# Kernel optimization log

Measured on AMD Instinct MI355X. Metric: run time of the kernel, lower is better.

The kernel has to match this reference:

```python
import jax, jax.numpy as jnp
import numpy as np

B, S, H, F, V, MAX_OOV = 128, 512, 1024, 512, 50000, 50


def setup_inputs() -> dict:
    key = jax.random.key(0)
    ks = jax.random.split(key, 20)
    r = lambda i, shp, s=0.02: (jax.random.normal(ks[i], shp, jnp.float32) * s)
    return dict(
        input=jax.random.randint(ks[0], (B,), 0, V),
        hidden=jax.random.normal(ks[1], (1, B, H), jnp.float32) * 0.1,
        encoder_outputs=jax.random.normal(ks[2], (B, S, H), jnp.float32) * 0.1,
        x_padding_masks=jnp.ones((B, S), jnp.float32),
        len_oov=jax.random.randint(ks[3], (B,), 0, MAX_OOV),
        coverage_vector=jnp.zeros((B, S), jnp.float32),
        ref2tgt=jax.random.randint(ks[4], (B, S), 0, V + MAX_OOV),
        emb=r(5, (V, F)),
        W_ih=r(6, (3 * H, F)), W_hh=r(7, (3 * H, H)),
        b_ih=jnp.zeros(3 * H, jnp.float32), b_hh=jnp.zeros(3 * H, jnp.float32),
        e2v1_w=r(8, (F, H)), e2v1_b=jnp.zeros(F, jnp.float32),
        e2v2_w=r(9, (V, F)), e2v2_b=jnp.zeros(V, jnp.float32),
        fc_w=r(10, (H, 2 * H)), fc_b=jnp.zeros(H, jnp.float32),
        wgen_w=r(11, (1, 2 * H + F)), wgen_b=jnp.zeros(1, jnp.float32),
        att_Wh=r(12, (H, H)), att_Ws=r(13, (H, H)),
        att_wc=r(14, (H,)), att_b=jnp.zeros(H, jnp.float32), att_v=r(15, (H,)),
    )


def reference(input, hidden, encoder_outputs, x_padding_masks, len_oov,
              coverage_vector, ref2tgt, emb, W_ih, W_hh, b_ih, b_hh,
              e2v1_w, e2v1_b, e2v2_w, e2v2_b, fc_w, fc_b, wgen_w, wgen_b,
              att_Wh, att_Ws, att_wc, att_b, att_v):
    # embedding lookup (dropout is identity at inference)
    emb_x = emb[input]  # [B, F]

    # --- additive (Bahdanau) attention with coverage ---
    s = hidden[0]  # [B, H] (n_layers == 1)
    feat = jnp.tanh(
        jnp.einsum('bsh,kh->bsk', encoder_outputs, att_Wh)
        + (s @ att_Ws.T)[:, None, :]
        + coverage_vector[:, :, None] * att_wc
        + att_b)  # [B, S, H]
    e = jnp.einsum('bsh,h->bs', feat, att_v)  # [B, S]
    a = jax.nn.softmax(e, axis=1) * x_padding_masks
    a = a / (jnp.sum(a, axis=1, keepdims=True))  # [B, S] renormalized attn
    coverage_new = coverage_vector + a
    context = jnp.einsum('bs,bsh->bh', a, encoder_outputs)  # [B, H]
    h_att = jnp.concatenate([s, context], axis=-1) @ fc_w.T + fc_b  # [B, H]

    # --- single-step GRU (PyTorch gate order r, z, n) ---
    gi = emb_x @ W_ih.T + b_ih  # [B, 3H]
    gh = h_att @ W_hh.T + b_hh  # [B, 3H]
    i_r, i_z, i_n = jnp.split(gi, 3, axis=-1)
    h_r, h_z, h_n = jnp.split(gh, 3, axis=-1)
    r = jax.nn.sigmoid(i_r + h_r)
    z = jax.nn.sigmoid(i_z + h_z)
    n = jnp.tanh(i_n + r * h_n)
    h_new = (1.0 - z) * n + z * h_att  # [B, H]

    # --- vocab distribution ---
    out1 = h_new @ e2v1_w.T + e2v1_b  # [B, F]
    p_vocab = jax.nn.softmax(out1 @ e2v2_w.T + e2v2_b, axis=1)  # [B, V]

    # --- pointer-generator mixing ---
    x_gen = jnp.concatenate([context, h_new, emb_x], axis=-1)  # [B, 2H+F]
    p_gen = jax.nn.sigmoid(x_gen @ wgen_w.T + wgen_b)[:, 0]  # [B]
    p_gen = jnp.clip(p_gen, 0.001, 0.999)
    p_vocab_w = p_gen[:, None] * p_vocab  # [B, V]
    attn_w = (1.0 - p_gen)[:, None] * a  # [B, S]
    p_ext = jnp.concatenate([p_vocab_w, jnp.zeros((B, MAX_OOV), p_vocab_w.dtype)], axis=1)
    rows = jnp.arange(B)[:, None]
    final = p_ext.at[rows, ref2tgt].add(attn_w)  # scatter_add over extended vocab

    return final, h_new[None], coverage_new, a
```

## Files before the change

### kernel.cpp

```cpp
#include <hip/hip_runtime.h>
#include <math.h>

#define B_   128
#define S_   512
#define H_   1024
#define F_   512
#define V_   50000
#define OOV_ 50
#define EV_  (V_ + OOV_)

#define BM 128
#define BN 128
#define BK 64

typedef __attribute__((ext_vector_type(8))) __bf16 bf16x8;
typedef __attribute__((ext_vector_type(4))) __bf16 bf16x4;
typedef __attribute__((ext_vector_type(4))) float  f32x4;

__device__ __forceinline__ void gload_lds16(const void* g, void* lds) {
  __builtin_amdgcn_global_load_lds(
      (const __attribute__((address_space(1))) unsigned int*)g,
      (__attribute__((address_space(3))) unsigned int*)lds, 16, 0, 0);
}

__device__ __forceinline__ float fast_tanh(float x) {
  float v = fminf(fmaxf(x, -15.f), 15.f);
  float t = __expf(2.f * v);
  return 1.f - 2.f / (t + 1.f);
}

__global__ __launch_bounds__(256)
void cast_both_kernel(const float* __restrict__ enc, __bf16* __restrict__ enc_h,
                      const float* __restrict__ wh, __bf16* __restrict__ wh_h)
{
  const size_t n_enc = (size_t)B_ * S_ * H_;
  const size_t n_tot = n_enc + (size_t)H_ * H_;
  for (size_t i = ((size_t)blockIdx.x * 256 + threadIdx.x) * 8; i < n_tot;
       i += (size_t)gridDim.x * 256 * 8) {
    const float* in; __bf16* out; size_t j;
    if (i < n_enc) { in = enc; out = enc_h; j = i; }
    else           { in = wh;  out = wh_h;  j = i - n_enc; }
    float4 a = *(const float4*)(in + j);
    float4 b = *(const float4*)(in + j + 4);
    bf16x8 o;
    o[0] = (__bf16)a.x; o[1] = (__bf16)a.y; o[2] = (__bf16)a.z; o[3] = (__bf16)a.w;
    o[4] = (__bf16)b.x; o[5] = (__bf16)b.y; o[6] = (__bf16)b.z; o[7] = (__bf16)b.w;
    *(bf16x8*)(out + j) = o;
  }
}

__global__ __launch_bounds__(256)
void gemm_splitk(const float* __restrict__ A, const float* __restrict__ W,
                 float* __restrict__ partial, int N, int K, int KS)
{
  __shared__ float As[128 * 68];
  __shared__ float Ws[32 * 68];
  const int tid = threadIdx.x;
  const int n0 = blockIdx.x * 32;
  const int p  = blockIdx.y;
  const int tx = tid & 7, ty = tid >> 3;
  const int lr = tid >> 4, lc4 = (tid & 15) * 4;
  float acc[4][4] = {};
  const int kend = p * KS + KS;
  for (int k0 = p * KS; k0 < kend; k0 += 64) {
#pragma unroll
    for (int pp = 0; pp < 8; ++pp)
      *(float4*)(As + (pp * 16 + lr) * 68 + lc4) =
          *(const float4*)(A + (size_t)(pp * 16 + lr) * K + k0 + lc4);
#pragma unroll
    for (int pp = 0; pp < 2; ++pp)
      *(float4*)(Ws + (pp * 16 + lr) * 68 + lc4) =
          *(const float4*)(W + (size_t)(n0 + pp * 16 + lr) * K + k0 + lc4);
    __syncthreads();
#pragma unroll
    for (int kk = 0; kk < 16; ++kk) {
      float4 av[4], wv[4];
#pragma unroll
      for (int i = 0; i < 4; i++) av[i] = *(const float4*)(As + (ty * 4 + i) * 68 + kk * 4);
#pragma unroll
      for (int j = 0; j < 4; j++) wv[j] = *(const float4*)(Ws + (tx * 4 + j) * 68 + kk * 4);
#pragma unroll
      for (int i = 0; i < 4; i++)
#pragma unroll
        for (int j = 0; j < 4; j++) {
          acc[i][j] = fmaf(av[i].x, wv[j].x, acc[i][j]);
          acc[i][j] = fmaf(av[i].y, wv[j].y, acc[i][j]);
          acc[i][j] = fmaf(av[i].z, wv[j].z, acc[i][j]);
          acc[i][j] = fmaf(av[i].w, wv[j].w, acc[i][j]);
        }
    }
    __syncthreads();
  }
#pragma unroll
  for (int i = 0; i < 4; i++)
#pragma unroll
    for (int j = 0; j < 4; j++)
      partial[((size_t)p * 128 + ty * 4 + i) * N + n0 + tx * 4 + j] = acc[i][j];
}

__global__ __launch_bounds__(256)
void gemm_splitk_cat(const float* __restrict__ A1, const float* __restrict__ A2,
                     const float* __restrict__ W, float* __restrict__ partial,
                     int N, int K, int KS)
{
  __shared__ float As[128 * 68];
  __shared__ float Ws[32 * 68];
  const int tid = threadIdx.x;
  const int n0 = blockIdx.x * 32;
  const int p  = blockIdx.y;
  const int tx = tid & 7, ty = tid >> 3;
  const int lr = tid >> 4, lc4 = (tid & 15) * 4;
  const float* A = (p * KS < 1024) ? A1 : A2;
  const int kbase = (p * KS < 1024) ? 0 : 1024;
  float acc[4][4] = {};
  const int kend = p * KS + KS;
  for (int k0 = p * KS; k0 < kend; k0 += 64) {
#pragma unroll
    for (int pp = 0; pp < 8; ++pp)
      *(float4*)(As + (pp * 16 + lr) * 68 + lc4) =
          *(const float4*)(A + (size_t)(pp * 16 + lr) * 1024 + (k0 - kbase) + lc4);
#pragma unroll
    for (int pp = 0; pp < 2; ++pp)
      *(float4*)(Ws + (pp * 16 + lr) * 68 + lc4) =
          *(const float4*)(W + (size_t)(n0 + pp * 16 + lr) * K + k0 + lc4);
    __syncthreads();
#pragma unroll
    for (int kk = 0; kk < 16; ++kk) {
      float4 av[4], wv[4];
#pragma unroll
      for (int i = 0; i < 4; i++) av[i] = *(const float4*)(As + (ty * 4 + i) * 68 + kk * 4);
#pragma unroll
      for (int j = 0; j < 4; j++) wv[j] = *(const float4*)(Ws + (tx * 4 + j) * 68 + kk * 4);
#pragma unroll
      for (int i = 0; i < 4; i++)
#pragma unroll
        for (int j = 0; j < 4; j++) {
          acc[i][j] = fmaf(av[i].x, wv[j].x, acc[i][j]);
          acc[i][j] = fmaf(av[i].y, wv[j].y, acc[i][j]);
          acc[i][j] = fmaf(av[i].z, wv[j].z, acc[i][j]);
          acc[i][j] = fmaf(av[i].w, wv[j].w, acc[i][j]);
        }
    }
    __syncthreads();
  }
#pragma unroll
  for (int i = 0; i < 4; i++)
#pragma unroll
    for (int j = 0; j < 4; j++)
      partial[((size_t)p * 128 + ty * 4 + i) * N + n0 + tx * 4 + j] = acc[i][j];
}

__global__ __launch_bounds__(256)
void gemm_splitk_gather(const int* __restrict__ input, const float* __restrict__ emb,
                        const float* __restrict__ W, float* __restrict__ partial,
                        int N, int K, int KS)
{
  __shared__ float As[128 * 68];
  __shared__ float Ws[32 * 68];
  const int tid = threadIdx.x;
  const int n0 = blockIdx.x * 32;
  const int p  = blockIdx.y;
  const int tx = tid & 7, ty = tid >> 3;
  const int lr = tid >> 4, lc4 = (tid & 15) * 4;
  float acc[4][4] = {};
  const int kend = p * KS + KS;
  for (int k0 = p * KS; k0 < kend; k0 += 64) {
#pragma unroll
    for (int pp = 0; pp < 8; ++pp) {
      int row = input[pp * 16 + lr];
      *(float4*)(As + (pp * 16 + lr) * 68 + lc4) =
          *(const float4*)(emb + (size_t)row * K + k0 + lc4);
    }
#pragma unroll
    for (int pp = 0; pp < 2; ++pp)
      *(float4*)(Ws + (pp * 16 + lr) * 68 + lc4) =
          *(const float4*)(W + (size_t)(n0 + pp * 16 + lr) * K + k0 + lc4);
    __syncthreads();
#pragma unroll
    for (int kk = 0; kk < 16; ++kk) {
      float4 av[4], wv[4];
#pragma unroll
      for (int i = 0; i < 4; i++) av[i] = *(const float4*)(As + (ty * 4 + i) * 68 + kk * 4);
#pragma unroll
      for (int j = 0; j < 4; j++) wv[j] = *(const float4*)(Ws + (tx * 4 + j) * 68 + kk * 4);
#pragma unroll
      for (int i = 0; i < 4; i++)
#pragma unroll
        for (int j = 0; j < 4; j++) {
          acc[i][j] = fmaf(av[i].x, wv[j].x, acc[i][j]);
          acc[i][j] = fmaf(av[i].y, wv[j].y, acc[i][j]);
          acc[i][j] = fmaf(av[i].z, wv[j].z, acc[i][j]);
          acc[i][j] = fmaf(av[i].w, wv[j].w, acc[i][j]);
        }
    }
    __syncthreads();
  }
#pragma unroll
  for (int i = 0; i < 4; i++)
#pragma unroll
    for (int j = 0; j < 4; j++)
      partial[((size_t)p * 128 + ty * 4 + i) * N + n0 + tx * 4 + j] = acc[i][j];
}

__global__ __launch_bounds__(256)
void reduce_partial(const float* __restrict__ partial, const float* __restrict__ bias,
                    float* __restrict__ C, int N, int P)
{
  int idx = blockIdx.x * 256 + threadIdx.x;
  int n = idx % N;
  float s = bias ? bias[n] : 0.f;
  for (int p = 0; p < P; ++p) s += partial[(size_t)p * 128 * N + idx];
  C[idx] = s;
}

__global__ __launch_bounds__(256)
void reduce_partial_bf16(const float* __restrict__ partial, const float* __restrict__ bias,
                         __bf16* __restrict__ C, int N, int P)
{
  int idx = blockIdx.x * 256 + threadIdx.x;
  int n = idx % N;
  float s = bias ? bias[n] : 0.f;
  for (int p = 0; p < P; ++p) s += partial[(size_t)p * 128 * N + idx];
  C[idx] = (__bf16)s;
}

__global__ __launch_bounds__(512, 1)
void feat_mfma256_kernel(const __bf16* __restrict__ enc, const __bf16* __restrict__ Wh,
                         const float* __restrict__ sws, const float* __restrict__ cov,
                         const float* __restrict__ wcv, const float* __restrict__ ab,
                         const float* __restrict__ av_, float* __restrict__ e_part)
{
  __shared__ __attribute__((aligned(16))) __bf16 As[2][2][128 * 64];
  __shared__ __attribute__((aligned(16))) __bf16 Bs[2][2][128 * 64];
  const int tid  = threadIdx.x;
  const int lane = tid & 63, wid = tid >> 6;
  const int wr = wid >> 2, wc = wid & 3;
  const int bid = blockIdx.x;
  const int swz = (bid & 7) * 128 + (bid >> 3);
  const int mt = swz >> 2, nt = swz & 3;
  const int bs0 = mt * 256;
  const int n0  = nt * 256;
  const int b   = bs0 >> 9;

  const int scb = ((tid & 7) * 16) ^ (((tid >> 3) & 7) << 4);
  const __bf16* aS[2][2];
  const __bf16* bS[2][2];
#pragma unroll
  for (int h = 0; h < 2; ++h)
#pragma unroll
    for (int q = 0; q < 2; ++q) {
      int r = h * 128 + q * 64 + (tid >> 3);
      aS[h][q] = enc + (size_t)(bs0 + r) * H_ + (scb >> 1);
      bS[h][q] = Wh  + (size_t)(n0  + r) * H_ + (scb >> 1);
    }
  const int ldsQ0 = tid * 16, ldsQ1 = 8192 + tid * 16;

  const int lrow = lane & 15, kbase = (lane >> 4) << 4;
  const int bh = wc >> 1;
  int aO[8][2], bO[4][2];
#pragma unroll
  for (int m = 0; m < 8; ++m) {
    int rh = m * 16 + lrow, sw = (rh & 7) << 4;
    aO[m][0] = rh * 128 + (kbase ^ sw);
    aO[m][1] = rh * 128 + ((64 + kbase) ^ sw);
  }
#pragma unroll
  for (int n = 0; n < 4; ++n) {
    int rh = (wc & 1) * 64 + n * 16 + lrow, sw = (rh & 7) << 4;
    bO[n][0] = rh * 128 + (kbase ^ sw);
    bO[n][1] = rh * 128 + ((64 + kbase) ^ sw);
  }

  f32x4 acc[8][4];
#pragma unroll
  for (int i = 0; i < 8; i++)
#pragma unroll
    for (int j = 0; j < 4; j++) acc[i][j] = (f32x4){0.f, 0.f, 0.f, 0.f};
  bf16x8 bfv[4][2];

#define STG_A(d, h, ofs)                                                       \
  { gload_lds16(aS[h][0] + (ofs), (char*)As[d][h] + ldsQ0);                    \
    gload_lds16(aS[h][1] + (ofs), (char*)As[d][h] + ldsQ1); }
#define STG_B(d, h, ofs)                                                       \
  { gload_lds16(bS[h][0] + (ofs), (char*)Bs[d][h] + ldsQ0);                    \
    gload_lds16(bS[h][1] + (ofs), (char*)Bs[d][h] + ldsQ1); }
#define BAR()                                                                  \
  { __builtin_amdgcn_sched_barrier(0); __builtin_amdgcn_s_barrier();           \
    __builtin_amdgcn_sched_barrier(0); }
#define LGKM0()                                                                \
  { asm volatile("s_waitcnt lgkmcnt(0)" ::: "memory");                         \
    __builtin_amdgcn_sched_barrier(0); }
#define VMC(n)                                                                 \
  { asm volatile("s_waitcnt vmcnt(" #n ")" ::: "memory");                      \
    __builtin_amdgcn_sched_barrier(0); }
#define RD_B(d)                                                                \
  { _Pragma("unroll")                                                          \
    for (int n = 0; n < 4; ++n) {                                              \
      bfv[n][0] = *(const bf16x8*)((const char*)Bs[d][bh] + bO[n][0]);         \
      bfv[n][1] = *(const bf16x8*)((const char*)Bs[d][bh] + bO[n][1]);         \
    } }
#define PH(d, q, STGSTMT, TAILWAIT)                                            \
  {                                                                            \
    bf16x8 x00 = *(const bf16x8*)((const char*)As[d][wr] + aO[2*(q)][0]);      \
    bf16x8 x01 = *(const bf16x8*)((const char*)As[d][wr] + aO[2*(q)][1]);      \
    bf16x8 x10 = *(const bf16x8*)((const char*)As[d][wr] + aO[2*(q)+1][0]);    \
    bf16x8 x11 = *(const bf16x8*)((const char*)As[d][wr] + aO[2*(q)+1][1]);    \
    STGSTMT;                                                                   \
    BAR(); LGKM0();                                                            \
    __builtin_amdgcn_s_setprio(1);                                             \
    _Pragma("unroll")                                                          \
    for (int n = 0; n < 4; ++n) {                                              \
      acc[2*(q)][n]   = __builtin_amdgcn_mfma_f32_16x16x32_bf16(x00, bfv[n][0], acc[2*(q)][n], 0, 0, 0);   \
      acc[2*(q)][n]   = __builtin_amdgcn_mfma_f32_16x16x32_bf16(x01, bfv[n][1], acc[2*(q)][n], 0, 0, 0);   \
      acc[2*(q)+1][n] = __builtin_amdgcn_mfma_f32_16x16x32_bf16(x10, bfv[n][0], acc[2*(q)+1][n], 0, 0, 0); \
      acc[2*(q)+1][n] = __builtin_amdgcn_mfma_f32_16x16x32_bf16(x11, bfv[n][1], acc[2*(q)+1][n], 0, 0, 0); \
    }                                                                          \
    __builtin_amdgcn_s_setprio(0);                                             \
    TAILWAIT; BAR();                                                           \
  }

  STG_B(0, 0, 0) STG_B(0, 1, 0) STG_A(0, 0, 0) STG_A(0, 1, 0)
  STG_B(1, 0, 64) STG_B(1, 1, 64)
  VMC(4); BAR();

#pragma unroll 1
  for (int i = 0; i < 7; ++i) {
    RD_B(0);
    PH(0, 0, STG_A(1, 0, 64), )
    PH(0, 1, STG_A(1, 1, 64), )
    PH(0, 2, STG_B(0, 0, 128), )
    PH(0, 3, STG_B(0, 1, 128), VMC(4))
    RD_B(1);
    PH(1, 0, STG_A(0, 0, 128), )
    PH(1, 1, STG_A(0, 1, 128), )
    PH(1, 2, STG_B(1, 0, 192), )
    PH(1, 3, STG_B(1, 1, 192), VMC(4))
#pragma unroll
    for (int h = 0; h < 2; ++h)
#pragma unroll
      for (int q = 0; q < 2; ++q) { aS[h][q] += 128; bS[h][q] += 128; }
  }
  RD_B(0);
  PH(0, 0, STG_A(1, 0, 64), )
  PH(0, 1, STG_A(1, 1, 64), )
  PH(0, 2, , )
  PH(0, 3, , VMC(0))
  RD_B(1);
  PH(1, 0, , )
  PH(1, 1, , )
  PH(1, 2, , )
  PH(1, 3, , )
  __syncthreads();
#undef STG_A
#undef STG_B
#undef BAR
#undef LGKM0
#undef VMC
#undef RD_B
#undef PH

  float rowsum[8][4];
#pragma unroll
  for (int m = 0; m < 8; m++)
#pragma unroll
    for (int j = 0; j < 4; j++) rowsum[m][j] = 0.f;

#pragma unroll
  for (int n = 0; n < 4; ++n) {
    int col_g = n0 + wc * 64 + n * 16 + (lane & 15);
    float sw   = sws[(size_t)b * H_ + col_g];
    float wc_n = wcv[col_g], ab_n = ab[col_g], av_n = av_[col_g];
#pragma unroll
    for (int m = 0; m < 8; ++m) {
#pragma unroll
      for (int j = 0; j < 4; ++j) {
        int row_l = wr * 128 + m * 16 + ((lane >> 4) << 2) + j;
        float val = acc[m][n][j] + sw + cov[bs0 + row_l] * wc_n + ab_n;
        rowsum[m][j] += fast_tanh(val) * av_n;
      }
    }
  }
#pragma unroll
  for (int m = 0; m < 8; ++m)
#pragma unroll
    for (int j = 0; j < 4; ++j) {
      float v = rowsum[m][j];
      v += __shfl_xor(v, 1);
      v += __shfl_xor(v, 2);
      v += __shfl_xor(v, 4);
      v += __shfl_xor(v, 8);
      rowsum[m][j] = v;
    }
  float (*red)[4] = (float(*)[4])As;
  if ((lane & 15) == 0) {
#pragma unroll
    for (int m = 0; m < 8; ++m)
#pragma unroll
      for (int j = 0; j < 4; ++j)
        red[wr * 128 + m * 16 + ((lane >> 4) << 2) + j][wc] = rowsum[m][j];
  }
  __syncthreads();
  if (tid < 256)
    e_part[(size_t)nt * (B_ * S_) + bs0 + tid] =
        red[tid][0] + red[tid][1] + red[tid][2] + red[tid][3];
}

__global__ __launch_bounds__(256)
void logits_mfma_kernel(const __bf16* __restrict__ A, const float* __restrict__ W,
                        const float* __restrict__ bias, float* __restrict__ out0)
{
  __shared__ __attribute__((aligned(16))) __bf16 As[BM * BK];
  __shared__ __attribute__((aligned(16))) __bf16 Bs[BN * BK];
  const int tid  = threadIdx.x;
  const int lane = tid & 63, wid = tid >> 6;
  const int wr = wid >> 1, wcc = wid & 1;
  const int n0 = blockIdx.x * BN;

  f32x4 acc[4][4];
#pragma unroll
  for (int i = 0; i < 4; i++)
#pragma unroll
    for (int j = 0; j < 4; j++) acc[i][j] = (f32x4){0.f, 0.f, 0.f, 0.f};

  for (int k0 = 0; k0 < F_; k0 += BK) {
#pragma unroll
    for (int p = 0; p < 4; ++p) {
      int off = p * 4096 + tid * 16;
      int r = off >> 7, cb = off & 127;
      int scb = cb ^ ((r & 7) << 4);
      gload_lds16(A + (size_t)r * F_ + k0 + (scb >> 1), (char*)As + off);
    }
#pragma unroll
    for (int p = 0; p < 8; ++p) {
      int idx = p * 1024 + tid * 4;
      int r = idx >> 6, c = idx & 63;
      int row_g = n0 + r; if (row_g >= V_) row_g = V_ - 1;
      float4 f = *(const float4*)(W + (size_t)row_g * F_ + k0 + c);
      union { __bf16 h[4]; uint2 u; } t;
      t.h[0] = (__bf16)f.x; t.h[1] = (__bf16)f.y; t.h[2] = (__bf16)f.z; t.h[3] = (__bf16)f.w;
      int cb = c * 2;
      *(uint2*)((char*)Bs + r * 128 + (cb ^ ((r & 7) << 4))) = t.u;
    }
    __syncthreads();

    bf16x8 af[4][2], bfv[4][2];
#pragma unroll
    for (int m = 0; m < 4; ++m) {
      int row = wr * 64 + m * 16 + (lane & 15);
      int swz = (row & 7) << 4;
#pragma unroll
      for (int kk = 0; kk < 2; ++kk) {
        int kb = kk * 64 + ((lane >> 4) << 4);
        af[m][kk] = *(const bf16x8*)((const char*)As + row * 128 + (kb ^ swz));
      }
    }
#pragma unroll
    for (int n = 0; n < 4; ++n) {
      int row = wcc * 64 + n * 16 + (lane & 15);
      int swz = (row & 7) << 4;
#pragma unroll
      for (int kk = 0; kk < 2; ++kk) {
        int kb = kk * 64 + ((lane >> 4) << 4);
        bfv[n][kk] = *(const bf16x8*)((const char*)Bs + row * 128 + (kb ^ swz));
      }
    }
#pragma unroll
    for (int m = 0; m < 4; ++m)
#pragma unroll
      for (int n = 0; n < 4; ++n)
#pragma unroll
        for (int kk = 0; kk < 2; ++kk)
          acc[m][n] = __builtin_amdgcn_mfma_f32_16x16x32_bf16(af[m][kk], bfv[n][kk], acc[m][n], 0, 0, 0);
    __syncthreads();
  }

#pragma unroll
  for (int m = 0; m < 4; ++m) {
#pragma unroll
    for (int n = 0; n < 4; ++n) {
      int col_g = n0 + wcc * 64 + n * 16 + (lane & 15);
      if (col_g >= V_) continue;
      float bv = bias[col_g];
#pragma unroll
      for (int j = 0; j < 4; ++j) {
        int row = wr * 64 + m * 16 + ((lane >> 4) << 2) + j;
        out0[(size_t)row * EV_ + col_g] = acc[m][n][j] + bv;
      }
    }
  }
}

__global__ __launch_bounds__(512)
void softmax_a_kernel(const float* __restrict__ e_part, const float* __restrict__ mask,
                      const float* __restrict__ cov, float* __restrict__ a_ws,
                      float* __restrict__ out_a, float* __restrict__ out_cov)
{
  const int b = blockIdx.x;
  const int s = threadIdx.x;
  __shared__ float red[512];
  float e = 0.f;
  for (int kt = 0; kt < 4; ++kt) e += e_part[(size_t)kt * (B_ * S_) + b * S_ + s];
  red[s] = e;
  __syncthreads();
  for (int st = 256; st > 0; st >>= 1) {
    if (s < st) red[s] = fmaxf(red[s], red[s + st]);
    __syncthreads();
  }
  float mx = red[0];
  __syncthreads();
  float ex = expf(e - mx) * mask[b * S_ + s];
  red[s] = ex;
  __syncthreads();
  for (int st = 256; st > 0; st >>= 1) {
    if (s < st) red[s] += red[s + st];
    __syncthreads();
  }
  float a = ex / red[0];
  a_ws[b * S_ + s] = a;
  out_a[b * S_ + s] = a;
  out_cov[b * S_ + s] = cov[b * S_ + s] + a;
}

__global__ __launch_bounds__(256)
void context_kernel(const float* __restrict__ a_ws, const __bf16* __restrict__ enc,
                    float* __restrict__ ctx)
{
  const int b = blockIdx.y, q = blockIdx.x;
  const int lane = threadIdx.x & 63, w = threadIdx.x >> 6;
  const int h0 = q * 256 + lane * 4;
  __shared__ float al[S_];
  __shared__ float part[4][256];
  for (int i = threadIdx.x; i < S_; i += 256) al[i] = a_ws[b * S_ + i];
  __syncthreads();
  float acc0 = 0.f, acc1 = 0.f, acc2 = 0.f, acc3 = 0.f;
  const __bf16* ep = enc + (size_t)b * S_ * H_ + h0;
#pragma unroll 4
  for (int s = w * 128; s < w * 128 + 128; ++s) {
    bf16x4 v = *(const bf16x4*)(ep + (size_t)s * H_);
    float a = al[s];
    acc0 = fmaf(a, (float)v[0], acc0);
    acc1 = fmaf(a, (float)v[1], acc1);
    acc2 = fmaf(a, (float)v[2], acc2);
    acc3 = fmaf(a, (float)v[3], acc3);
  }
  part[w][lane * 4 + 0] = acc0;
  part[w][lane * 4 + 1] = acc1;
  part[w][lane * 4 + 2] = acc2;
  part[w][lane * 4 + 3] = acc3;
  __syncthreads();
  if (threadIdx.x < 256) {
    int o = threadIdx.x;
    ctx[b * H_ + q * 256 + o] = part[0][o] + part[1][o] + part[2][o] + part[3][o];
  }
}

__global__ __launch_bounds__(256)
void gru_kernel(const float* __restrict__ pgi, const float* __restrict__ pgh,
                const float* __restrict__ b_ih, const float* __restrict__ b_hh,
                const float* __restrict__ h_att, float* __restrict__ h_new_ws,
                float* __restrict__ out_h)
{
  int idx = blockIdx.x * 256 + threadIdx.x;
  int b = idx >> 10, h = idx & 1023;
  float ir = b_ih[h], iz = b_ih[H_ + h], in_ = b_ih[2 * H_ + h];
  float hr = b_hh[h], hz = b_hh[H_ + h], hn = b_hh[2 * H_ + h];
#pragma unroll
  for (int p = 0; p < 8; ++p) {
    const float* gp = pgi + (size_t)p * 128 * 3072 + (size_t)b * 3072;
    ir += gp[h]; iz += gp[H_ + h]; in_ += gp[2 * H_ + h];
    const float* hp = pgh + (size_t)p * 128 * 3072 + (size_t)b * 3072;
    hr += hp[h]; hz += hp[H_ + h]; hn += hp[2 * H_ + h];
  }
  float r = 1.f / (1.f + expf(-(ir + hr)));
  float z = 1.f / (1.f + expf(-(iz + hz)));
  float n = tanhf(in_ + r * hn);
  float ha = h_att[(size_t)b * H_ + h];
  float hv = (1.f - z) * n + z * ha;
  h_new_ws[idx] = hv;
  out_h[idx] = hv;
}

__global__ __launch_bounds__(512)
void stats_pgen_kernel(const float* __restrict__ logits, float* __restrict__ vmax,
                       float* __restrict__ vsum, const float* __restrict__ context,
                       const float* __restrict__ h_new, const int* __restrict__ input,
                       const float* __restrict__ emb, const float* __restrict__ wgen_w,
                       const float* __restrict__ wgen_b, float* __restrict__ pgen)
{
  __shared__ float red[512];
  if (blockIdx.x < B_) {
    int b = blockIdx.x;
    const float* row = logits + (size_t)b * EV_;
    float m = -1e30f;
    for (int v = threadIdx.x; v < V_; v += 512) m = fmaxf(m, row[v]);
    red[threadIdx.x] = m;
    __syncthreads();
    for (int st = 256; st > 0; st >>= 1) {
      if (threadIdx.x < st) red[threadIdx.x] = fmaxf(red[threadIdx.x], red[threadIdx.x + st]);
      __syncthreads();
    }
    m = red[0];
    __syncthreads();
    float ssum = 0.f;
    for (int v = threadIdx.x; v < V_; v += 512) ssum += expf(row[v] - m);
    red[threadIdx.x] = ssum;
    __syncthreads();
    for (int st = 256; st > 0; st >>= 1) {
      if (threadIdx.x < st) red[threadIdx.x] += red[threadIdx.x + st];
      __syncthreads();
    }
    if (threadIdx.x == 0) { vmax[b] = m; vsum[b] = red[0]; }
  } else {
    int b = blockIdx.x - B_;
    const float* erow = emb + (size_t)input[b] * F_;
    float acc = 0.f;
    for (int j = threadIdx.x; j < H_; j += 512) acc = fmaf(context[b * H_ + j], wgen_w[j], acc);
    for (int j = threadIdx.x; j < H_; j += 512) acc = fmaf(h_new[b * H_ + j], wgen_w[H_ + j], acc);
    for (int j = threadIdx.x; j < F_; j += 512) acc = fmaf(erow[j], wgen_w[2 * H_ + j], acc);
    red[threadIdx.x] = acc;
    __syncthreads();
    for (int st = 256; st > 0; st >>= 1) {
      if (threadIdx.x < st) red[threadIdx.x] += red[threadIdx.x + st];
      __syncthreads();
    }
    if (threadIdx.x == 0) {
      float p = 1.f / (1.f + expf(-(red[0] + wgen_b[0])));
      p = fminf(fmaxf(p, 0.001f), 0.999f);
      pgen[b] = p;
    }
  }
}

__global__ void final_kernel(float* __restrict__ out0, const float* __restrict__ vmax,
                             const float* __restrict__ vsum, const float* __restrict__ pgen)
{
  int b = blockIdx.y;
  int v = blockIdx.x * 256 + threadIdx.x;
  if (v >= EV_) return;
  float* row = out0 + (size_t)b * EV_;
  if (v < V_) row[v] = pgen[b] * expf(row[v] - vmax[b]) / vsum[b];
  else row[v] = 0.f;
}

__global__ void scatter_kernel(const int* __restrict__ ref2tgt, const float* __restrict__ a_ws,
                               const float* __restrict__ pgen, float* __restrict__ out0)
{
  int b = blockIdx.x;
  int s = threadIdx.x;
  float w = (1.f - pgen[b]) * a_ws[b * S_ + s];
  int t = ref2tgt[b * S_ + s];
  atomicAdd(&out0[(size_t)b * EV_ + t], w);
}

extern "C" void kernel_launch(void* const* d_in, const int* in_sizes, int n_in,
                              void* d_out, int out_size, void* d_ws, size_t ws_size,
                              hipStream_t stream)
{
  const int*   input   = (const int*)d_in[0];
  const float* hidden  = (const float*)d_in[1];
  const float* enc     = (const float*)d_in[2];
  const float* mask    = (const float*)d_in[3];
  const float* cov     = (const float*)d_in[5];
  const int*   ref2tgt = (const int*)d_in[6];
  const float* emb     = (const float*)d_in[7];
  const float* W_ih    = (const float*)d_in[8];
  const float* W_hh    = (const float*)d_in[9];
  const float* b_ih    = (const float*)d_in[10];
  const float* b_hh    = (const float*)d_in[11];
  const float* e2v1_w  = (const float*)d_in[12];
  const float* e2v1_b  = (const float*)d_in[13];
  const float* e2v2_w  = (const float*)d_in[14];
  const float* e2v2_b  = (const float*)d_in[15];
  const float* fc_w    = (const float*)d_in[16];
  const float* fc_b    = (const float*)d_in[17];
  const float* wgen_w  = (const float*)d_in[18];
  const float* wgen_b  = (const float*)d_in[19];
  const float* att_Wh  = (const float*)d_in[20];
  const float* att_Ws  = (const float*)d_in[21];
  const float* att_wc  = (const float*)d_in[22];
  const float* att_b   = (const float*)d_in[23];
  const float* att_v   = (const float*)d_in[24];

  char* w = (char*)d_ws;
  __bf16* enc_h  = (__bf16*)w;  w += (size_t)B_ * S_ * H_ * 2;
  __bf16* Wh_h   = (__bf16*)w;  w += (size_t)H_ * H_ * 2;
  __bf16* out1_h = (__bf16*)w;  w += (size_t)B_ * F_ * 2;
  float* sws     = (float*)w;   w += (size_t)B_ * H_ * 4;
  float* e_part  = (float*)w;   w += (size_t)8 * B_ * S_ * 4;
  float* a_ws    = (float*)w;   w += (size_t)B_ * S_ * 4;
  float* context = (float*)w;   w += (size_t)B_ * H_ * 4;
  float* h_att   = (float*)w;   w += (size_t)B_ * H_ * 4;
  float* h_new   = (float*)w;   w += (size_t)B_ * H_ * 4;
  float* pgen    = (float*)w;   w += 128 * 4;
  float* vmax    = (float*)w;   w += 128 * 4;
  float* vsum    = (float*)w;   w += 128 * 4;
  float* pA      = (float*)w;   w += (size_t)16 * 128 * 1024 * 4;
  float* pB      = (float*)w;   w += (size_t)8 * 128 * 3072 * 4;
  float* pC      = (float*)w;   w += (size_t)8 * 128 * 3072 * 4;

  float* out0    = (float*)d_out;
  float* out_h   = out0 + (size_t)B_ * EV_;
  float* out_cov = out_h + (size_t)B_ * H_;
  float* out_a   = out_cov + (size_t)B_ * S_;

  cast_both_kernel<<<4096, 256, 0, stream>>>(enc, enc_h, att_Wh, Wh_h);
  gemm_splitk<<<dim3(32, 16), 256, 0, stream>>>(hidden, att_Ws, pA, H_, H_, 64);
  reduce_partial<<<512, 256, 0, stream>>>(pA, nullptr, sws, H_, 16);
  feat_mfma256_kernel<<<dim3(1024), 512, 0, stream>>>(enc_h, Wh_h, sws, cov, att_wc, att_b, att_v, e_part);
  softmax_a_kernel<<<B_, 512, 0, stream>>>(e_part, mask, cov, a_ws, out_a, out_cov);
  context_kernel<<<dim3(4, B_), 256, 0, stream>>>(a_ws, enc_h, context);
  gemm_splitk_cat<<<dim3(32, 16), 256, 0, stream>>>(hidden, context, fc_w, pA, H_, 2 * H_, 128);
  reduce_partial<<<512, 256, 0, stream>>>(pA, fc_b, h_att, H_, 16);
  gemm_splitk_gather<<<dim3(96, 8), 256, 0, stream>>>(input, emb, W_ih, pB, 3 * H_, F_, 64);
  gemm_splitk<<<dim3(96, 8), 256, 0, stream>>>(h_att, W_hh, pC, 3 * H_, H_, 128);
  gru_kernel<<<(B_ * H_) / 256, 256, 0, stream>>>(pB, pC, b_ih, b_hh, h_att, h_new, out_h);
  gemm_splitk<<<dim3(16, 16), 256, 0, stream>>>(h_new, e2v1_w, pA, F_, H_, 64);
  reduce_partial_bf16<<<256, 256, 0, stream>>>(pA, e2v1_b, out1_h, F_, 16);
  logits_mfma_kernel<<<dim3((V_ + BN - 1) / BN), 256, 0, stream>>>(out1_h, e2v2_w, e2v2_b, out0);
  stats_pgen_kernel<<<2 * B_, 512, 0, stream>>>(out0, vmax, vsum, context, h_new, input, emb,
                                                wgen_w, wgen_b, pgen);
  final_kernel<<<dim3((EV_ + 255) / 256, B_), 256, 0, stream>>>(out0, vmax, vsum, pgen);
  scatter_kernel<<<B_, 512, 0, stream>>>(ref2tgt, a_ws, pgen, out0);
}
```

Before: 461.1 us.

## Fuse cast and input GEMMs into front kernel, prefetch logits weights

Merges the bf16 cast, the s@Ws GEMM and the embedding@W_ih GEMM into one launch, with the GEMMs run without split-K so their reduce passes and partial buffers go away. The logits kernel now prefetches the next weight tile into registers while computing the current one. The stats loops read float2 vectors. These cut launch count and partial traffic, but the non-split GEMM blocks run the full K serially and may become a tail behind the cast blocks. The e_part buffer also shrinks from 8 to 4 partials, which depends on how feat_mfma256_kernel writes it.

```diff
diff --git a/kernel.cpp b/kernel.cpp
--- a/kernel.cpp
+++ b/kernel.cpp
@@ -30,23 +30,83 @@
 }
 
 __global__ __launch_bounds__(256)
-void cast_both_kernel(const float* __restrict__ enc, __bf16* __restrict__ enc_h,
-                      const float* __restrict__ wh, __bf16* __restrict__ wh_h)
-{
-  const size_t n_enc = (size_t)B_ * S_ * H_;
-  const size_t n_tot = n_enc + (size_t)H_ * H_;
-  for (size_t i = ((size_t)blockIdx.x * 256 + threadIdx.x) * 8; i < n_tot;
-       i += (size_t)gridDim.x * 256 * 8) {
-    const float* in; __bf16* out; size_t j;
-    if (i < n_enc) { in = enc; out = enc_h; j = i; }
-    else           { in = wh;  out = wh_h;  j = i - n_enc; }
-    float4 a = *(const float4*)(in + j);
-    float4 b = *(const float4*)(in + j + 4);
-    bf16x8 o;
-    o[0] = (__bf16)a.x; o[1] = (__bf16)a.y; o[2] = (__bf16)a.z; o[3] = (__bf16)a.w;
-    o[4] = (__bf16)b.x; o[5] = (__bf16)b.y; o[6] = (__bf16)b.z; o[7] = (__bf16)b.w;
-    *(bf16x8*)(out + j) = o;
-  }
+void front_kernel(const float* __restrict__ enc, __bf16* __restrict__ enc_h,
+                  const float* __restrict__ wh, __bf16* __restrict__ wh_h,
+                  const float* __restrict__ hidden, const float* __restrict__ att_Ws,
+                  float* __restrict__ sws, const int* __restrict__ input,
+                  const float* __restrict__ emb, const float* __restrict__ W_ih,
+                  float* __restrict__ gi)
+{
+  __shared__ float As[128 * 68];
+  __shared__ float Ws[32 * 68];
+  const int bid = blockIdx.x;
+  const int tid = threadIdx.x;
+  if (bid < 4096) {
+    const size_t n_enc = (size_t)B_ * S_ * H_;
+    const size_t n_tot = n_enc + (size_t)H_ * H_;
+    for (size_t i = ((size_t)bid * 256 + tid) * 8; i < n_tot;
+         i += (size_t)4096 * 256 * 8) {
+      const float* in; __bf16* out; size_t j;
+      if (i < n_enc) { in = enc; out = enc_h; j = i; }
+      else           { in = wh;  out = wh_h;  j = i - n_enc; }
+      float4 a = *(const float4*)(in + j);
+      float4 b = *(const float4*)(in + j + 4);
+      bf16x8 o;
+      o[0] = (__bf16)a.x; o[1] = (__bf16)a.y; o[2] = (__bf16)a.z; o[3] = (__bf16)a.w;
+      o[4] = (__bf16)b.x; o[5] = (__bf16)b.y; o[6] = (__bf16)b.z; o[7] = (__bf16)b.w;
+      *(bf16x8*)(out + j) = o;
+    }
+    return;
+  }
+  const int sel = (bid >= 4128) ? 1 : 0;
+  const int n0  = sel ? (bid - 4128) * 32 : (bid - 4096) * 32;
+  const int N   = sel ? 3 * H_ : H_;
+  const int K   = sel ? F_ : H_;
+  const float* Wm = sel ? W_ih : att_Ws;
+  float* outp = sel ? gi : sws;
+  const int tx = tid & 7, ty = tid >> 3;
+  const int lr = tid >> 4, lc4 = (tid & 15) * 4;
+  const float* arow[8];
+#pragma unroll
+  for (int pp = 0; pp < 8; ++pp) {
+    int m = pp * 16 + lr;
+    if (sel) arow[pp] = emb + (size_t)input[m] * F_;
+    else     arow[pp] = hidden + (size_t)m * H_;
+  }
+  float acc[4][4] = {};
+  for (int k0 = 0; k0 < K; k0 += 64) {
+#pragma unroll
+    for (int pp = 0; pp < 8; ++pp)
+      *(float4*)(As + (pp * 16 + lr) * 68 + lc4) = *(const float4*)(arow[pp] + k0 + lc4);
+#pragma unroll
+    for (int pp = 0; pp < 2; ++pp)
+      *(float4*)(Ws + (pp * 16 + lr) * 68 + lc4) =
+          *(const float4*)(Wm + (size_t)(n0 + pp * 16 + lr) * K + k0 + lc4);
+    __syncthreads();
+#pragma unroll
+    for (int kk = 0; kk < 16; ++kk) {
+      float4 av[4], wv[4];
+#pragma unroll
+      for (int i = 0; i < 4; i++) av[i] = *(const float4*)(As + (ty * 4 + i) * 68 + kk * 4);
+#pragma unroll
+      for (int j = 0; j < 4; j++) wv[j] = *(const float4*)(Ws + (tx * 4 + j) * 68 + kk * 4);
+#pragma unroll
+      for (int i = 0; i < 4; i++)
+#pragma unroll
+        for (int j = 0; j < 4; j++) {
+          acc[i][j] = fmaf(av[i].x, wv[j].x, acc[i][j]);
+          acc[i][j] = fmaf(av[i].y, wv[j].y, acc[i][j]);
+          acc[i][j] = fmaf(av[i].z, wv[j].z, acc[i][j]);
+          acc[i][j] = fmaf(av[i].w, wv[j].w, acc[i][j]);
+        }
+    }
+    __syncthreads();
+  }
+#pragma unroll
+  for (int i = 0; i < 4; i++)
+#pragma unroll
+    for (int j = 0; j < 4; j++)
+      outp[(size_t)(ty * 4 + i) * N + n0 + tx * 4 + j] = acc[i][j];
 }
 
 __global__ __launch_bounds__(256)
@@ -119,58 +179,6 @@
     for (int pp = 0; pp < 8; ++pp)
       *(float4*)(As + (pp * 16 + lr) * 68 + lc4) =
           *(const float4*)(A + (size_t)(pp * 16 + lr) * 1024 + (k0 - kbase) + lc4);
-#pragma unroll
-    for (int pp = 0; pp < 2; ++pp)
-      *(float4*)(Ws + (pp * 16 + lr) * 68 + lc4) =
-          *(const float4*)(W + (size_t)(n0 + pp * 16 + lr) * K + k0 + lc4);
-    __syncthreads();
-#pragma unroll
-    for (int kk = 0; kk < 16; ++kk) {
-      float4 av[4], wv[4];
-#pragma unroll
-      for (int i = 0; i < 4; i++) av[i] = *(const float4*)(As + (ty * 4 + i) * 68 + kk * 4);
-#pragma unroll
-      for (int j = 0; j < 4; j++) wv[j] = *(const float4*)(Ws + (tx * 4 + j) * 68 + kk * 4);
-#pragma unroll
-      for (int i = 0; i < 4; i++)
-#pragma unroll
-        for (int j = 0; j < 4; j++) {
-          acc[i][j] = fmaf(av[i].x, wv[j].x, acc[i][j]);
-          acc[i][j] = fmaf(av[i].y, wv[j].y, acc[i][j]);
-          acc[i][j] = fmaf(av[i].z, wv[j].z, acc[i][j]);
-          acc[i][j] = fmaf(av[i].w, wv[j].w, acc[i][j]);
-        }
-    }
-    __syncthreads();
-  }
-#pragma unroll
-  for (int i = 0; i < 4; i++)
-#pragma unroll
-    for (int j = 0; j < 4; j++)
-      partial[((size_t)p * 128 + ty * 4 + i) * N + n0 + tx * 4 + j] = acc[i][j];
-}
-
-__global__ __launch_bounds__(256)
-void gemm_splitk_gather(const int* __restrict__ input, const float* __restrict__ emb,
-                        const float* __restrict__ W, float* __restrict__ partial,
-                        int N, int K, int KS)
-{
-  __shared__ float As[128 * 68];
-  __shared__ float Ws[32 * 68];
-  const int tid = threadIdx.x;
-  const int n0 = blockIdx.x * 32;
-  const int p  = blockIdx.y;
-  const int tx = tid & 7, ty = tid >> 3;
-  const int lr = tid >> 4, lc4 = (tid & 15) * 4;
-  float acc[4][4] = {};
-  const int kend = p * KS + KS;
-  for (int k0 = p * KS; k0 < kend; k0 += 64) {
-#pragma unroll
-    for (int pp = 0; pp < 8; ++pp) {
-      int row = input[pp * 16 + lr];
-      *(float4*)(As + (pp * 16 + lr) * 68 + lc4) =
-          *(const float4*)(emb + (size_t)row * K + k0 + lc4);
-    }
 #pragma unroll
     for (int pp = 0; pp < 2; ++pp)
       *(float4*)(Ws + (pp * 16 + lr) * 68 + lc4) =
@@ -422,6 +430,20 @@
 #pragma unroll
     for (int j = 0; j < 4; j++) acc[i][j] = (f32x4){0.f, 0.f, 0.f, 0.f};
 
+  const float* wsrc[8];
+  int wdst[8];
+#pragma unroll
+  for (int p = 0; p < 8; ++p) {
+    int idx = p * 1024 + tid * 4;
+    int r = idx >> 6, c = idx & 63;
+    int row_g = n0 + r; if (row_g >= V_) row_g = V_ - 1;
+    wsrc[p] = W + (size_t)row_g * F_ + c;
+    wdst[p] = r * 128 + ((c * 2) ^ ((r & 7) << 4));
+  }
+  float4 wreg[8];
+#pragma unroll
+  for (int p = 0; p < 8; ++p) wreg[p] = *(const float4*)(wsrc[p]);
+
   for (int k0 = 0; k0 < F_; k0 += BK) {
 #pragma unroll
     for (int p = 0; p < 4; ++p) {
@@ -432,16 +454,16 @@
     }
 #pragma unroll
     for (int p = 0; p < 8; ++p) {
-      int idx = p * 1024 + tid * 4;
-      int r = idx >> 6, c = idx & 63;
-      int row_g = n0 + r; if (row_g >= V_) row_g = V_ - 1;
-      float4 f = *(const float4*)(W + (size_t)row_g * F_ + k0 + c);
       union { __bf16 h[4]; uint2 u; } t;
-      t.h[0] = (__bf16)f.x; t.h[1] = (__bf16)f.y; t.h[2] = (__bf16)f.z; t.h[3] = (__bf16)f.w;
-      int cb = c * 2;
-      *(uint2*)((char*)Bs + r * 128 + (cb ^ ((r & 7) << 4))) = t.u;
-    }
-    __syncthreads();
+      t.h[0] = (__bf16)wreg[p].x; t.h[1] = (__bf16)wreg[p].y;
+      t.h[2] = (__bf16)wreg[p].z; t.h[3] = (__bf16)wreg[p].w;
+      *(uint2*)((char*)Bs + wdst[p]) = t.u;
+    }
+    __syncthreads();
+    if (k0 + BK < F_) {
+#pragma unroll
+      for (int p = 0; p < 8; ++p) wreg[p] = *(const float4*)(wsrc[p] + k0 + BK);
+    }
 
     bf16x8 af[4][2], bfv[4][2];
 #pragma unroll
@@ -555,19 +577,20 @@
 }
 
 __global__ __launch_bounds__(256)
-void gru_kernel(const float* __restrict__ pgi, const float* __restrict__ pgh,
+void gru_kernel(const float* __restrict__ gi, const float* __restrict__ pgh,
                 const float* __restrict__ b_ih, const float* __restrict__ b_hh,
                 const float* __restrict__ h_att, float* __restrict__ h_new_ws,
                 float* __restrict__ out_h)
 {
   int idx = blockIdx.x * 256 + threadIdx.x;
   int b = idx >> 10, h = idx & 1023;
-  float ir = b_ih[h], iz = b_ih[H_ + h], in_ = b_ih[2 * H_ + h];
+  const float* gp = gi + (size_t)b * 3072;
+  float ir = b_ih[h] + gp[h];
+  float iz = b_ih[H_ + h] + gp[H_ + h];
+  float in_ = b_ih[2 * H_ + h] + gp[2 * H_ + h];
   float hr = b_hh[h], hz = b_hh[H_ + h], hn = b_hh[2 * H_ + h];
 #pragma unroll
   for (int p = 0; p < 8; ++p) {
-    const float* gp = pgi + (size_t)p * 128 * 3072 + (size_t)b * 3072;
-    ir += gp[h]; iz += gp[H_ + h]; in_ += gp[2 * H_ + h];
     const float* hp = pgh + (size_t)p * 128 * 3072 + (size_t)b * 3072;
     hr += hp[h]; hz += hp[H_ + h]; hn += hp[2 * H_ + h];
   }
@@ -592,7 +615,10 @@
     int b = blockIdx.x;
     const float* row = logits + (size_t)b * EV_;
     float m = -1e30f;
-    for (int v = threadIdx.x; v < V_; v += 512) m = fmaxf(m, row[v]);
+    for (int v = threadIdx.x * 2; v < V_; v += 1024) {
+      float2 x = *(const float2*)(row + v);
+      m = fmaxf(m, fmaxf(x.x, x.y));
+    }
     red[threadIdx.x] = m;
     __syncthreads();
     for (int st = 256; st > 0; st >>= 1) {
@@ -602,7 +628,10 @@
     m = red[0];
     __syncthreads();
     float ssum = 0.f;
-    for (int v = threadIdx.x; v < V_; v += 512) ssum += expf(row[v] - m);
+    for (int v = threadIdx.x * 2; v < V_; v += 1024) {
+      float2 x = *(const float2*)(row + v);
+      ssum += expf(x.x - m) + expf(x.y - m);
+    }
     red[threadIdx.x] = ssum;
     __syncthreads();
     for (int st = 256; st > 0; st >>= 1) {
@@ -686,7 +715,8 @@
   __bf16* Wh_h   = (__bf16*)w;  w += (size_t)H_ * H_ * 2;
   __bf16* out1_h = (__bf16*)w;  w += (size_t)B_ * F_ * 2;
   float* sws     = (float*)w;   w += (size_t)B_ * H_ * 4;
-  float* e_part  = (float*)w;   w += (size_t)8 * B_ * S_ * 4;
+  float* gi      = (float*)w;   w += (size_t)B_ * 3 * H_ * 4;
+  float* e_part  = (float*)w;   w += (size_t)4 * B_ * S_ * 4;
   float* a_ws    = (float*)w;   w += (size_t)B_ * S_ * 4;
   float* context = (float*)w;   w += (size_t)B_ * H_ * 4;
   float* h_att   = (float*)w;   w += (size_t)B_ * H_ * 4;
@@ -695,7 +725,6 @@
   float* vmax    = (float*)w;   w += 128 * 4;
   float* vsum    = (float*)w;   w += 128 * 4;
   float* pA      = (float*)w;   w += (size_t)16 * 128 * 1024 * 4;
-  float* pB      = (float*)w;   w += (size_t)8 * 128 * 3072 * 4;
   float* pC      = (float*)w;   w += (size_t)8 * 128 * 3072 * 4;
 
   float* out0    = (float*)d_out;
@@ -703,17 +732,15 @@
   float* out_cov = out_h + (size_t)B_ * H_;
   float* out_a   = out_cov + (size_t)B_ * S_;
 
-  cast_both_kernel<<<4096, 256, 0, stream>>>(enc, enc_h, att_Wh, Wh_h);
-  gemm_splitk<<<dim3(32, 16), 256, 0, stream>>>(hidden, att_Ws, pA, H_, H_, 64);
-  reduce_partial<<<512, 256, 0, stream>>>(pA, nullptr, sws, H_, 16);
+  front_kernel<<<4224, 256, 0, stream>>>(enc, enc_h, att_Wh, Wh_h,
+                                         hidden, att_Ws, sws, input, emb, W_ih, gi);
   feat_mfma256_kernel<<<dim3(1024), 512, 0, stream>>>(enc_h, Wh_h, sws, cov, att_wc, att_b, att_v, e_part);
   softmax_a_kernel<<<B_, 512, 0, stream>>>(e_part, mask, cov, a_ws, out_a, out_cov);
   context_kernel<<<dim3(4, B_), 256, 0, stream>>>(a_ws, enc_h, context);
   gemm_splitk_cat<<<dim3(32, 16), 256, 0, stream>>>(hidden, context, fc_w, pA, H_, 2 * H_, 128);
   reduce_partial<<<512, 256, 0, stream>>>(pA, fc_b, h_att, H_, 16);
-  gemm_splitk_gather<<<dim3(96, 8), 256, 0, stream>>>(input, emb, W_ih, pB, 3 * H_, F_, 64);
   gemm_splitk<<<dim3(96, 8), 256, 0, stream>>>(h_att, W_hh, pC, 3 * H_, H_, 128);
-  gru_kernel<<<(B_ * H_) / 256, 256, 0, stream>>>(pB, pC, b_ih, b_hh, h_att, h_new, out_h);
+  gru_kernel<<<(B_ * H_) / 256, 256, 0, stream>>>(gi, pC, b_ih, b_hh, h_att, h_new, out_h);
   gemm_splitk<<<dim3(16, 16), 256, 0, stream>>>(h_new, e2v1_w, pA, F_, H_, 64);
   reduce_partial_bf16<<<256, 256, 0, stream>>>(pA, e2v1_b, out1_h, F_, 16);
   logits_mfma_kernel<<<dim3((V_ + BN - 1) / BN), 256, 0, stream>>>(out1_h, e2v2_w, e2v2_b, out0);
```

Result: slower. 490.4 us (+6.4%).
